# Kernel tuning notes

Hardware: AMD Instinct MI355X
Metric: run time of the kernel (lower is better)

Reference implementation:

```python
import jax, jax.numpy as jnp
import numpy as np
import math

E, NNODE = 32768, 2048          # edges, nodes
NUM_SPECIES, EMB = 100, 32
MUL, HIDDEN, N_RBF, LMAX, ENV_P = 16, 256, 8, 3, 6
SL = {0: slice(0, 1), 1: slice(1, 4), 2: slice(4, 9), 3: slice(9, 16)}  # SH blocks


def _cg(j1, m1, j2, m2, j3, m3):
    """Clebsch-Gordan coefficient (Racah formula), complex SH basis."""
    if m1 + m2 != m3:
        return 0.0
    f = math.factorial
    pre = math.sqrt((2*j3+1) * f(j1+j2-j3) * f(j1-j2+j3) * f(-j1+j2+j3) / f(j1+j2+j3+1))
    pre *= math.sqrt(f(j3+m3)*f(j3-m3)*f(j1-m1)*f(j1+m1)*f(j2-m2)*f(j2+m2))
    s = 0.0
    kmin = max(0, j2 - j3 - m1, j1 - j3 + m2)
    kmax = min(j1 + j2 - j3, j1 - m1, j2 + m2)
    for k in range(kmin, kmax + 1):
        s += (-1)**k / (f(k)*f(j1+j2-j3-k)*f(j1-m1-k)*f(j2+m2-k)*f(j3-j2+m1+k)*f(j3-j1-m2+k))
    return pre * s


def _umat(l):
    """Complex->real spherical-harmonics change of basis."""
    U = np.zeros((2*l+1, 2*l+1), dtype=complex)
    U[l, l] = 1.0
    s2 = 1.0 / math.sqrt(2.0)
    for m in range(1, l + 1):
        U[l+m, l-m] = s2
        U[l+m, l+m] = (-1)**m * s2
        U[l-m, l-m] = 1j * s2
        U[l-m, l+m] = -1j * (-1)**m * s2
    return U


def _real_coupling(l1, l2, l3):
    """Real-basis CG coupling tensor, Frobenius-normalized (w3j analogue)."""
    C = np.zeros((2*l1+1, 2*l2+1, 2*l3+1), dtype=complex)
    for a, m1 in enumerate(range(-l1, l1+1)):
        for b, m2 in enumerate(range(-l2, l2+1)):
            for c, m3 in enumerate(range(-l3, l3+1)):
                C[a, b, c] = _cg(l1, m1, l2, m2, l3, m3)
    T = np.einsum('am,bn,ck,mnk->abc', _umat(l1), _umat(l2), _umat(l3).conj(), C)
    Tr, Ti = np.real(T), np.imag(T)
    T = Tr if np.linalg.norm(Tr) >= np.linalg.norm(Ti) else Ti
    n = np.linalg.norm(T)
    return None if n < 1e-8 else (T / n).astype(np.float32)


PATHS = {l3: [] for l3 in range(LMAX + 1)}
for _l1 in range(LMAX + 1):
    for _l2 in range(LMAX + 1):
        for _l3 in range(abs(_l1 - _l2), min(_l1 + _l2, LMAX) + 1):
            _T = _real_coupling(_l1, _l2, _l3)
            if _T is not None:
                PATHS[_l3].append((_l1, _l2, jnp.asarray(_T)))
NPATH = {l3: len(PATHS[l3]) for l3 in range(LMAX + 1)}


def envelope(d):  # polynomial smoothing envelope, p=6, cutoff=1
    p = ENV_P
    e = 1.0 - 0.5*(p+1)*(p+2)*d**p + p*(p+2)*d**(p+1) - 0.5*p*(p+1)*d**(p+2)
    return jnp.where(d < 1.0, e, 0.0)


def bessel(d):  # radial Bessel basis [E] -> [E, N_RBF]
    n = jnp.arange(1, N_RBF + 1, dtype=d.dtype)
    ds = jnp.where(d == 0.0, 1.0, d)[:, None]
    return (math.sqrt(2.0) * jnp.sin(n * jnp.pi * ds) / ds) * envelope(d)[:, None]


def sph_harm16(u):  # real SH l=0..3, component norm (|Y_l|^2 = 2l+1), [E,16]
    x, y, z = u[:, 0], u[:, 1], u[:, 2]
    x2, y2, z2 = x*x, y*y, z*z
    s3, s15, s5 = math.sqrt(3.0), math.sqrt(15.0), math.sqrt(5.0)
    s358, s105 = math.sqrt(35.0/8.0), math.sqrt(105.0)
    s218, s7 = math.sqrt(21.0/8.0), math.sqrt(7.0)
    return jnp.stack([
        jnp.ones_like(x),
        s3*y, s3*z, s3*x,
        s15*x*y, s15*y*z, 0.5*s5*(3*z2 - 1), s15*x*z, 0.5*s15*(x2 - y2),
        s358*y*(3*x2 - y2), s105*x*y*z, s218*y*(5*z2 - 1), 0.5*s7*(5*z2 - 3)*z,
        s218*x*(5*z2 - 1), 0.5*s105*(x2 - y2)*z, s358*x*(x2 - y2),
    ], axis=1)


def dense(x, W):  # e3nn-style bias-free linear, 1/sqrt(fan_in)
    return (x @ W) / math.sqrt(W.shape[0])


def dense_axis(V, W):  # [E,C,K] x [C,D] -> [E,D,K]
    return jnp.einsum('eck,cd->edk', V, W) / math.sqrt(W.shape[0])


def tensor_product(A, B, lmax_out):
    """CG tensor product [E,MUL,16] x [E,MUL,16] -> {l3: [E,MUL*npath,2l3+1]}."""
    out = {}
    for l3 in range(lmax_out + 1):
        scale = math.sqrt(2*l3 + 1)
        parts = [scale * jnp.einsum('ijk,emi,emj->emk', T, A[:, :, SL[l1]], B[:, :, SL[l2]])
                 for (l1, l2, T) in PATHS[l3]]
        out[l3] = jnp.concatenate(parts, axis=1)
    return out


def allegro_layer(x, V, Y, senders, eps, env, alpha, Ww, Wl, Wv):
    w = dense(x, Ww)                                          # [E,MUL]
    node = jax.ops.segment_sum(w[:, :, None] * Y[:, None, :], senders, num_segments=NNODE)
    wY = node[senders] * eps                                  # scatter_sum + map_back
    lmax_out = LMAX if Wv is not None else 0
    tp = tensor_product(wY, V, lmax_out)
    xc = jnp.concatenate([x, tp[0][:, :, 0]], axis=1)         # fold 0e into scalars
    h = jax.nn.silu(dense(xc, Wl[0]))
    h = jax.nn.silu(dense(h, Wl[1]))
    y = env[:, None] * dense(h, Wl[2])
    a2 = alpha**2
    x = (x + a2 * y) / (1.0 + a2)
    if Wv is None:
        return x, None
    Vn = jnp.concatenate(
        [jnp.zeros((V.shape[0], MUL, 1), x.dtype)] +           # no 0e in output irreps
        [dense_axis(tp[l], Wv[l - 1]) for l in (1, 2, 3)], axis=2)
    return x, Vn


def _forward(vectors, varepsilon, alpha, emb, W_tb1, W_tb2, W_tb3, W_tb4,
             W_w0, W_w1, W_l11, W_l12, W_l13, W_v1, W_v2, W_v3,
             W_w2, W_l21, W_l22, W_l23, W_h, W_out,
             senders, receivers, species):
    d = jnp.linalg.norm(vectors, axis=1)
    u = vectors / jnp.where(d == 0.0, 1.0, d)[:, None]
    env = envelope(d)
    eps = 1.0 / jnp.sqrt(1.0 + varepsilon**2)
    x = jnp.concatenate([bessel(d), emb[species[senders]], emb[species[receivers]]], axis=1)
    x = jnp.where(d[:, None] == 0.0, 0.0, x)
    x = jax.nn.silu(dense(x, W_tb1))
    x = jax.nn.silu(dense(x, W_tb2))
    x = jax.nn.silu(dense(x, W_tb3))
    x = dense(x, W_tb4)
    x = env[:, None] * x                                      # [E,HIDDEN]
    Y = sph_harm16(u)                                         # [E,16]
    V = dense(x, W_w0)[:, :, None] * Y[:, None, :]            # [E,MUL,16]
    x, V = allegro_layer(x, V, Y, senders, eps, env, alpha,
                         W_w1, (W_l11, W_l12, W_l13), (W_v1, W_v2, W_v3))
    x, _ = allegro_layer(x, V, Y, senders, eps, env, alpha,
                         W_w2, (W_l21, W_l22, W_l23), None)
    x = dense(x, W_h)
    return env[:, None] * dense(x, W_out)                     # [E,1]


def setup_inputs():
    key = jax.random.key(0)
    ks = jax.random.split(key, 32)
    dirs = jax.random.normal(ks[0], (E, 3), dtype=jnp.float32)
    dirs = dirs / jnp.linalg.norm(dirs, axis=1, keepdims=True)
    r = jax.random.uniform(ks[1], (E, 1), minval=0.05, maxval=0.95, dtype=jnp.float32)
    w = lambda k, s: jax.random.normal(k, s, dtype=jnp.float32)
    n0 = NPATH[0]
    return {
        "vectors": dirs * r,
        "varepsilon": jnp.asarray(4.0, jnp.float32),   # sqrt(avg_num_neighbors=16)
        "alpha": jnp.asarray(1.0, jnp.float32),
        "emb": w(ks[5], (NUM_SPECIES, EMB)),
        "W_tb1": w(ks[6], (N_RBF + 2*EMB, HIDDEN // 8)),
        "W_tb2": w(ks[7], (HIDDEN // 8, HIDDEN // 4)),
        "W_tb3": w(ks[8], (HIDDEN // 4, HIDDEN // 2)),
        "W_tb4": w(ks[9], (HIDDEN // 2, HIDDEN)),
        "W_w0": w(ks[10], (HIDDEN, MUL)),
        "W_w1": w(ks[11], (HIDDEN, MUL)),
        "W_l11": w(ks[12], (HIDDEN + MUL * n0, HIDDEN)),
        "W_l12": w(ks[13], (HIDDEN, HIDDEN)),
        "W_l13": w(ks[14], (HIDDEN, HIDDEN)),
        "W_v1": w(ks[15], (MUL * NPATH[1], MUL)),
        "W_v2": w(ks[16], (MUL * NPATH[2], MUL)),
        "W_v3": w(ks[17], (MUL * NPATH[3], MUL)),
        "W_w2": w(ks[18], (HIDDEN, MUL)),
        "W_l21": w(ks[19], (HIDDEN + MUL * n0, HIDDEN)),
        "W_l22": w(ks[20], (HIDDEN, HIDDEN)),
        "W_l23": w(ks[21], (HIDDEN, HIDDEN)),
        "W_h": w(ks[22], (HIDDEN, 128)),
        "W_out": w(ks[23], (128, 1)),
        "senders": jax.random.randint(ks[2], (E,), 0, NNODE),
        "receivers": jax.random.randint(ks[3], (E,), 0, NNODE),
        "species": jax.random.randint(ks[4], (NNODE,), 0, NUM_SPECIES),
    }


def reference(vectors, varepsilon, alpha, emb, W_tb1, W_tb2, W_tb3, W_tb4,
              W_w0, W_w1, W_l11, W_l12, W_l13, W_v1, W_v2, W_v3,
              W_w2, W_l21, W_l22, W_l23, W_h, W_out,
              senders, receivers, species):
    return _forward(vectors, varepsilon, alpha, emb, W_tb1, W_tb2, W_tb3, W_tb4,
                    W_w0, W_w1, W_l11, W_l12, W_l13, W_v1, W_v2, W_v3,
                    W_w2, W_l21, W_l22, W_l23, W_h, W_out,
                    senders, receivers, species)
```

## Files before the change

kernel.cpp:

```cpp
#include <hip/hip_runtime.h>
#include <cmath>
#include <complex>
#include <cstdio>
#include <cstring>
#include <algorithm>

#define E_EDGES 32768
#define NNODES  2048
#define VN_E    128

namespace cgt {

static double fct(int n){
  static const double f[13] = {1.,1.,2.,6.,24.,120.,720.,5040.,40320.,362880.,
                               3628800.,39916800.,479001600.};
  return f[n];
}

static double cg(int j1,int m1,int j2,int m2,int j3,int m3){
  if (m1+m2 != m3) return 0.0;
  double pre = std::sqrt((2*j3+1)*fct(j1+j2-j3)*fct(j1-j2+j3)*fct(-j1+j2+j3)/fct(j1+j2+j3+1));
  pre *= std::sqrt(fct(j3+m3)*fct(j3-m3)*fct(j1-m1)*fct(j1+m1)*fct(j2-m2)*fct(j2+m2));
  int kmin = 0;
  if (j2-j3-m1 > kmin) kmin = j2-j3-m1;
// ... 301 lines not shown
        int row = mrow + r4 + r;
        HsA[row*264 + j*16 + fr] = f2h(silu(acc[j][r]*rs));
      }
    __syncthreads();
  }

  {
    f32x4 acc[16] = {};
    for (int k0 = 0; k0 < 128; k0 += 32) {
#pragma unroll
      for (int h = 0; h < 2; h++) {
        int n = h*128 + srb;
        const unsigned short* s = Wt4 + (size_t)n*128 + k0 + skb;
        uint4 u0 = *(const uint4*)s;
        uint4 u1 = *(const uint4*)(s + 8);
        *(uint4*)((char*)BsB + swz(n, skb))     = u0;
        *(uint4*)((char*)BsB + swz(n, skb + 8)) = u1;
      }
      __syncthreads();
      half8 af = *(half8*)(HsA + (mrow + fr)*264 + k0 + fk);
#pragma unroll
      for (int j = 0; j < 16; j++) {
        half8 bf = *(half8*)((char*)BsB + swz(j*16 + fr, fk));
        acc[j] = MFMA16(af, bf, acc[j], 0, 0, 0);
      }
      __syncthreads();
    }
    const float rs = 0.08838834764831845f;
#pragma unroll
    for (int j = 0; j < 16; j++)
#pragma unroll
      for (int r = 0; r < 4; r++) {
        int row = mrow + r4 + r;
        float v = acc[j][r]*rs*envb[bm + row];
        unsigned short hv = f2h(v);
        HsB[row*264 + j*16 + fr] = hv;
        Xout[((size_t)(bm + row))*256 + j*16 + fr] = hv;
      }
    __syncthreads();
  }

  {
    f32x4 acc[2] = {};
    for (int k0 = 0; k0 < 256; k0 += 32) {
      if (tid < 64) {
        int n = tid >> 1, kb = (tid & 1) * 16;
        const unsigned short* s = Wt01 + (size_t)n*256 + k0 + kb;
        uint4 u0 = *(const uint4*)s;
        uint4 u1 = *(const uint4*)(s + 8);
        *(uint4*)((char*)BsB + swz(n, kb))     = u0;
        *(uint4*)((char*)BsB + swz(n, kb + 8)) = u1;
      }
      __syncthreads();
      half8 af = *(half8*)(HsB + (mrow + fr)*264 + k0 + fk);
      half8 b0 = *(half8*)((char*)BsB + swz(fr, fk));
      half8 b1 = *(half8*)((char*)BsB + swz(16 + fr, fk));
      acc[0] = MFMA16(af, b0, acc[0], 0, 0, 0);
      acc[1] = MFMA16(af, b1, acc[1], 0, 0, 0);
      __syncthreads();
    }
#pragma unroll
    for (int r = 0; r < 4; r++) {
      int row = mrow + r4 + r;
      w0s[row*16 + fr] = acc[0][r]*0.0625f;
      wb[((size_t)(bm + row))*16 + fr] = acc[1][r]*0.0625f;
    }
    __syncthreads();
  }

  for (int i = tid; i < 64*256; i += 256) {
    int e = i >> 8, idx = i & 255;
    V[(((size_t)(bm + e)) << 8) + idx] =
        f2h(w0s[e*16 + (idx & 15)] * Yb[(bm + e)*16 + (idx >> 4)]);
  }
}

template<int MODE>
__global__ __launch_bounds__(512) void mlp3_k(
    const unsigned short* __restrict__ X, const unsigned short* __restrict__ T0,
    const unsigned short* __restrict__ W1t, const unsigned short* __restrict__ W2t,
    const unsigned short* __restrict__ W3t, unsigned short* __restrict__ Out,
    const float* __restrict__ env, const float* __restrict__ alphap,
    const unsigned short* __restrict__ Wtw2, float* __restrict__ wb,
    const float* __restrict__ hc, float* __restrict__ outE)
{
  __shared__ unsigned short AsB[128*32];
  __shared__ unsigned short BsB[256*32];
  __shared__ unsigned short Hs[128*264];
  __shared__ float hcs[256];
  __shared__ float red[512];
  const int tid  = threadIdx.x;
  const int wave = tid >> 6, lane = tid & 63;
  const int bm = blockIdx.x*128;
  const int rowh = (wave >> 2)*64;
  const int wc = (wave & 3)*64;
  const int fr = lane & 15, fk = (lane >> 4) * 8;
  const int r4 = (lane >> 4) << 2;
  const int sra = tid >> 2, ska = (tid & 3) * 8;
  const int srb = tid >> 1, skb = (tid & 1) * 16;
  if (MODE == 1 && tid < 256) hcs[tid] = hc[tid];
  f32x4 acc[4][4] = {};

  for (int k0 = 0; k0 < 320; k0 += 32) {
    {
      int kk = k0 + ska;
      const unsigned short* ap = (kk < 256)
        ? X  + (size_t)(bm + sra)*256 + kk
        : T0 + (size_t)(bm + sra)*64  + (kk - 256);
      *(uint4*)((char*)AsB + swz(sra, ska)) = *(const uint4*)ap;
    }
    {
      const unsigned short* s = W1t + (size_t)srb*320 + k0 + skb;
      *(uint4*)((char*)BsB + swz(srb, skb))     = *(const uint4*)s;
      *(uint4*)((char*)BsB + swz(srb, skb + 8)) = *(const uint4*)(s + 8);
    }
    __syncthreads();
    half8 af[4], bf[4];
#pragma unroll
    for (int i = 0; i < 4; i++)
      af[i] = *(half8*)((char*)AsB + swz(rowh + i*16 + fr, fk));
#pragma unroll
    for (int j = 0; j < 4; j++)
      bf[j] = *(half8*)((char*)BsB + swz(wc + j*16 + fr, fk));
#pragma unroll
    for (int i = 0; i < 4; i++)
#pragma unroll
      for (int j = 0; j < 4; j++)
        acc[i][j] = MFMA16(af[i], bf[j], acc[i][j], 0, 0, 0);
    __syncthreads();
  }
  const float rs320 = 0.055901699437494740f;
#pragma unroll
  for (int i = 0; i < 4; i++)
#pragma unroll
    for (int r = 0; r < 4; r++) {
      int row = rowh + i*16 + r4 + r;
#pragma unroll
      for (int j = 0; j < 4; j++) {
        Hs[row*264 + wc + j*16 + fr] = f2h(silu(acc[i][j][r]*rs320));
        acc[i][j][r] = 0.f;
      }
    }
  __syncthreads();

  for (int k0 = 0; k0 < 256; k0 += 32) {
    {
      const unsigned short* s = W2t + (size_t)srb*256 + k0 + skb;
      *(uint4*)((char*)BsB + swz(srb, skb))     = *(const uint4*)s;
      *(uint4*)((char*)BsB + swz(srb, skb + 8)) = *(const uint4*)(s + 8);
    }
    __syncthreads();
    half8 af[4], bf[4];
#pragma unroll
    for (int i = 0; i < 4; i++)
      af[i] = *(half8*)(Hs + (rowh + i*16 + fr)*264 + k0 + fk);
#pragma unroll
    for (int j = 0; j < 4; j++)
      bf[j] = *(half8*)((char*)BsB + swz(wc + j*16 + fr, fk));
#pragma unroll
    for (int i = 0; i < 4; i++)
#pragma unroll
      for (int j = 0; j < 4; j++)
        acc[i][j] = MFMA16(af[i], bf[j], acc[i][j], 0, 0, 0);
    __syncthreads();
  }
#pragma unroll
  for (int i = 0; i < 4; i++)
#pragma unroll
    for (int r = 0; r < 4; r++) {
      int row = rowh + i*16 + r4 + r;
#pragma unroll
      for (int j = 0; j < 4; j++) {
        Hs[row*264 + wc + j*16 + fr] = f2h(silu(acc[i][j][r]*0.0625f));
        acc[i][j][r] = 0.f;
      }
    }
  __syncthreads();

  for (int k0 = 0; k0 < 256; k0 += 32) {
    {
      const unsigned short* s = W3t + (size_t)srb*256 + k0 + skb;
      *(uint4*)((char*)BsB + swz(srb, skb))     = *(const uint4*)s;
      *(uint4*)((char*)BsB + swz(srb, skb + 8)) = *(const uint4*)(s + 8);
    }
    __syncthreads();
    half8 af[4], bf[4];
#pragma unroll
    for (int i = 0; i < 4; i++)
      af[i] = *(half8*)(Hs + (rowh + i*16 + fr)*264 + k0 + fk);
#pragma unroll
    for (int j = 0; j < 4; j++)
      bf[j] = *(half8*)((char*)BsB + swz(wc + j*16 + fr, fk));
#pragma unroll
    for (int i = 0; i < 4; i++)
#pragma unroll
      for (int j = 0; j < 4; j++)
        acc[i][j] = MFMA16(af[i], bf[j], acc[i][j], 0, 0, 0);
    __syncthreads();
  }
  {
    float al = alphap[0];
    float a2 = al*al, inv1a2 = 1.f/(1.f+a2);
#pragma unroll
    for (int i = 0; i < 4; i++)
#pragma unroll
      for (int r = 0; r < 4; r++) {
        int row = rowh + i*16 + r4 + r;
        int grow = bm + row;
        float ev = env[grow];
#pragma unroll
        for (int j = 0; j < 4; j++) {
          int col = wc + j*16 + fr;
          float v = acc[i][j][r]*0.0625f*ev;
          v = (h2f(X[(size_t)grow*256 + col]) + a2*v)*inv1a2;
          unsigned short hv = f2h(v);
          Hs[row*264 + col] = hv;
          if (MODE == 0) Out[(size_t)grow*256 + col] = hv;
        }
      }
  }
  __syncthreads();

  if (MODE == 0) {
    f32x4 acc2[4] = {};
    for (int k0 = 0; k0 < 256; k0 += 32) {
      if (tid < 32) {
        int n = tid >> 1, kb = (tid & 1) * 16;
        const unsigned short* s = Wtw2 + (size_t)n*256 + k0 + kb;
        *(uint4*)((char*)BsB + swz(n, kb))     = *(const uint4*)s;
        *(uint4*)((char*)BsB + swz(n, kb + 8)) = *(const uint4*)(s + 8);
      }
      __syncthreads();
      if ((wave & 3) == 0) {
        half8 bf = *(half8*)((char*)BsB + swz(fr, fk));
#pragma unroll
        for (int i = 0; i < 4; i++) {
          half8 af = *(half8*)(Hs + (rowh + i*16 + fr)*264 + k0 + fk);
          acc2[i] = MFMA16(af, bf, acc2[i], 0, 0, 0);
        }
      }
      __syncthreads();
    }
    if ((wave & 3) == 0) {
#pragma unroll
      for (int i = 0; i < 4; i++)
#pragma unroll
        for (int r = 0; r < 4; r++)
          wb[((size_t)(bm + rowh + i*16 + r4 + r))*16 + fr] = acc2[i][r]*0.0625f;
    }
  } else {
    int row = tid >> 2, q = tid & 3;
    float p = 0.f;
#pragma unroll 16
    for (int c = q*64; c < q*64 + 64; c++)
      p += h2f(Hs[row*264 + c]) * hcs[c];
    red[tid] = p;
    __syncthreads();
    if (q == 0) {
      float t = red[tid] + red[tid+1] + red[tid+2] + red[tid+3];
      outE[bm + row] = env[bm + row]*t*0.0055242717280199023f;
    }
  }
}

__global__ __launch_bounds__(512) void vn_k(
    const float* __restrict__ node, const unsigned short* __restrict__ V,
    const int* __restrict__ senders, const float* __restrict__ varepsp,
    const int* __restrict__ pairsG, const unsigned short* __restrict__ Gtt,
    unsigned short* __restrict__ Vn, int Kdim,
    const int* __restrict__ pmeta, const int* __restrict__ entIJ,
    const float* __restrict__ entVal, unsigned short* __restrict__ tp0)
{
  __shared__ unsigned short Ab[VN_E*264];
  __shared__ unsigned short Bb[VN_E*264];
  __shared__ int Ps[256];
  const int tid = threadIdx.x;
  const int e0 = blockIdx.x * VN_E;
  const int wave = tid >> 6, lane = tid & 63;
  float ve = varepsp[0];
  float eps = rsqrtf(1.f + ve*ve);
  if (tid < 256) Ps[tid] = pairsG[tid];
#pragma unroll
  for (int rr = 0; rr < 16; rr++) {
    int row = wave*16 + rr;
    int s = senders[e0 + row];
    float4 fa = *(const float4*)(node + ((size_t)s << 8) + 4*lane);
    uint2 ub = *(const uint2*)(V + (((size_t)(e0 + row)) << 8) + 4*lane);
    unsigned short* ad = Ab + row*264 + 4*lane;
    unsigned short* bd = Bb + row*264 + 4*lane;
    uint2 ua;
    ua.x = (unsigned)f2h(fa.x*eps) | ((unsigned)f2h(fa.y*eps) << 16);
    ua.y = (unsigned)f2h(fa.z*eps) | ((unsigned)f2h(fa.w*eps) << 16);
    *(uint2*)ad = ua;
    *(uint2*)bd = ub;
  }
  __syncthreads();
  for (int o = tid; o < VN_E*64; o += 512) {
    int e = o >> 6, c = o & 63;
    int p = c >> 4, m = c & 15;
    const unsigned short* Ae = Ab + e*264;
    const unsigned short* Be = Bb + e*264;
    int es = pmeta[p*4+1], ec = pmeta[p*4+2];
    float acc = 0.f;
    for (int t = 0; t < ec; t++) {
      int ij = entIJ[es+t];
      acc += entVal[es+t] * h2f(Ae[((ij&255)<<4)+m]) * h2f(Be[(((ij>>8)&255)<<4)+m]);
    }
    tp0[((size_t)(e0+e)<<6) + pmeta[p*4+0] + m] = f2h(acc);
  }
  const int rowb = (wave & 1) * 64;
  const int wc   = (wave >> 1) * 64;
  const int fr = lane & 15, fk = (lane >> 4) * 8;
  const int pairSel = fk >> 4;
  const int moff = fk & 15;
  const int nslab = Kdim >> 5;
  f32x4 acc[4][4] = {};

  const unsigned short* Ar0 = Ab + (rowb + fr)*264;
  const unsigned short* Br0 = Bb + (rowb + fr)*264;
  const unsigned short* Ar1 = Ab + (rowb + 16 + fr)*264;
  const unsigned short* Br1 = Bb + (rowb + 16 + fr)*264;
  const unsigned short* Ar2 = Ab + (rowb + 32 + fr)*264;
  const unsigned short* Br2 = Bb + (rowb + 32 + fr)*264;
  const unsigned short* Ar3 = Ab + (rowb + 48 + fr)*264;
  const unsigned short* Br3 = Bb + (rowb + 48 + fr)*264;

// ... 27 lines not shown
    half8 a1 = rA1 * rB1;
    half8 a2 = rA2 * rB2;
    half8 a3 = rA3 * rB3;
    if (sl + 1 < nslab) {
      int pn = Ps[2*(sl + 1) + pairSel];
      int aoffn = ((pn & 255) << 4) + moff;
      int boffn = (((pn >> 8) & 255) << 4) + moff;
      rA0 = *(const half8*)(Ar0 + aoffn);
      rB0 = *(const half8*)(Br0 + boffn);
      rA1 = *(const half8*)(Ar1 + aoffn);
      rB1 = *(const half8*)(Br1 + boffn);
      rA2 = *(const half8*)(Ar2 + aoffn);
      rB2 = *(const half8*)(Br2 + boffn);
      rA3 = *(const half8*)(Ar3 + aoffn);
      rB3 = *(const half8*)(Br3 + boffn);
    }
    half8 d0, d1, d2, d3;
    if (sl + 2 < nslab) {
      const unsigned short* gn = gp + (size_t)(sl + 2) * 8192;
      d0 = *(const half8*)(gn);
      d1 = *(const half8*)(gn + 512);
      d2 = *(const half8*)(gn + 1024);
      d3 = *(const half8*)(gn + 1536);
    } else { d0 = c0; d1 = c1; d2 = c2; d3 = c3; }
    acc[0][0] = MFMA16(a0, b0, acc[0][0], 0, 0, 0);
    acc[1][0] = MFMA16(a1, b0, acc[1][0], 0, 0, 0);
    acc[2][0] = MFMA16(a2, b0, acc[2][0], 0, 0, 0);
    acc[3][0] = MFMA16(a3, b0, acc[3][0], 0, 0, 0);
    acc[0][1] = MFMA16(a0, b1, acc[0][1], 0, 0, 0);
    acc[1][1] = MFMA16(a1, b1, acc[1][1], 0, 0, 0);
    acc[2][1] = MFMA16(a2, b1, acc[2][1], 0, 0, 0);
    acc[3][1] = MFMA16(a3, b1, acc[3][1], 0, 0, 0);
    acc[0][2] = MFMA16(a0, b2, acc[0][2], 0, 0, 0);
    acc[1][2] = MFMA16(a1, b2, acc[1][2], 0, 0, 0);
    acc[2][2] = MFMA16(a2, b2, acc[2][2], 0, 0, 0);
    acc[3][2] = MFMA16(a3, b2, acc[3][2], 0, 0, 0);
    acc[0][3] = MFMA16(a0, b3, acc[0][3], 0, 0, 0);
    acc[1][3] = MFMA16(a1, b3, acc[1][3], 0, 0, 0);
    acc[2][3] = MFMA16(a2, b3, acc[2][3], 0, 0, 0);
    acc[3][3] = MFMA16(a3, b3, acc[3][3], 0, 0, 0);
    b0 = c0; b1 = c1; b2 = c2; b3 = c3;
    c0 = d0; c1 = d1; c2 = d2; c3 = d3;
  }
  const int r4 = (lane >> 4) << 2;
#pragma unroll
  for (int rg = 0; rg < 4; rg++) {
#pragma unroll
    for (int j = 0; j < 4; j++) {
#pragma unroll
      for (int r = 0; r < 4; r++) {
        int row = e0 + rowb + rg*16 + r4 + r;
        int col = wc + j*16 + fr;
        Vn[(size_t)row*256 + col] = f2h(acc[rg][j][r]);
      }
    }
  }
}

__global__ void gbuild_k(const float* __restrict__ TD,
    const float* __restrict__ Wv1, const float* __restrict__ Wv2,
    const float* __restrict__ Wv3, const int* __restrict__ sl_origc,
    unsigned short* __restrict__ Gt, int Kdim, int npairs,
    int s1b, int s1e, int s2e, int s3e)
{
  int k = blockIdx.x*256 + threadIdx.x;
  if (k >= Kdim) return;
  int col = blockIdx.y;
  int pair = k >> 4, m = k & 15;
  int d = col & 15, kabs = col >> 4;
  float acc = 0.f;
  if (kabs > 0 && pair < npairs) {
    const float* Wv; int ss, se, kloc;
    if (kabs < 4)      { Wv = Wv1; ss = s1b; se = s1e; kloc = kabs - 1; }
    else if (kabs < 9) { Wv = Wv2; ss = s1e; se = s2e; kloc = kabs - 4; }
    else               { Wv = Wv3; ss = s2e; se = s3e; kloc = kabs - 9; }
    for (int slot = ss; slot < se; slot++)
      acc += TD[((pair*30) + (slot - 4))*8 + kloc] * Wv[(sl_origc[slot] + m)*16 + d];
    acc *= rsqrtf((float)(16*(se - ss)));
  }
  Gt[((size_t)((k >> 5)*256 + col))*32 + (k & 31)] = f2h(acc);
}

struct WDesc { const float* src; unsigned short* dst; int K; int lgN; };
struct WPack { WDesc d[11]; };
__global__ void wcvt_k(WPack p){
  WDesc d = p.d[blockIdx.y];
  int total = d.K << d.lgN;
  int gid = blockIdx.x*256 + threadIdx.x;
  if (gid >= total) return;
  int k = gid >> d.lgN, n = gid & ((1 << d.lgN) - 1);
  d.dst[(size_t)n*d.K + k] = f2h(d.src[gid]);
}

__global__ void wcvt01_k(const float* __restrict__ W0, const float* __restrict__ W1,
                         unsigned short* __restrict__ dst){
  int gid = blockIdx.x*256 + threadIdx.x;
  int k = gid >> 5, n = gid & 31;
  float v = (n < 16) ? W0[k*16 + n] : W1[k*16 + (n - 16)];
  dst[(size_t)n*256 + k] = f2h(v);
}

__global__ void whc_k(const float* __restrict__ Wh, const float* __restrict__ Wout,
                      float* __restrict__ hc)
{
  int k = threadIdx.x;
  float s = 0.f;
#pragma unroll 16
  for (int j = 0; j < 128; j++) s += Wh[k*128 + j] * Wout[j];
  hc[k] = s;
}

__global__ void edge_init_k(const float* __restrict__ vectors, const int* __restrict__ senders,
    const int* __restrict__ receivers, const int* __restrict__ species,
    const float* __restrict__ emb, float* __restrict__ envb, float* __restrict__ Yb,
    float* __restrict__ x72)
{
  const int e = blockIdx.x*256 + threadIdx.x;
  float vx = vectors[e*3+0], vy = vectors[e*3+1], vz = vectors[e*3+2];
  float d = sqrtf(vx*vx+vy*vy+vz*vz);
  float dd = (d==0.f) ? 1.f : d;
  float invd = 1.f/dd;
  float x = vx*invd, y = vy*invd, z = vz*invd;
  float d2=d*d, d3=d2*d, d6=d3*d3, d7=d6*d, d8=d7*d;
  float envv = (d<1.f) ? (1.f - 28.f*d6 + 48.f*d7 - 21.f*d8) : 0.f;
  envb[e] = envv;
  float mask = (d==0.f)?0.f:1.f;
  const float SQ2 = 1.41421356237309515f;
  const float PIf = 3.14159265358979323846f;
  float* xr = x72 + (size_t)e*72;
#pragma unroll
  for (int n=1;n<=8;n++)
    xr[n-1] = SQ2 * sinf((float)n*PIf*dd)*invd*envv*mask;
  int sp_s = species[senders[e]], sp_r = species[receivers[e]];
  const float* es_ = emb + (size_t)sp_s*32;
  const float* er_ = emb + (size_t)sp_r*32;
#pragma unroll 8
  for (int k=0;k<32;k++){ xr[8+k] = es_[k]*mask; xr[40+k] = er_[k]*mask; }
  float x2=x*x, y2=y*y, z2=z*z;
  const float s3=1.7320508075688772f, s15=3.872983346207417f, s5=2.23606797749979f;
  const float s358=2.0916500663351889f, s105=10.246950765959598f;
  const float s218=1.6201851746019651f, s7=2.6457513110645907f;
  float* Yr = Yb + ((size_t)e<<4);
  Yr[0]=1.f;           Yr[1]=s3*y;          Yr[2]=s3*z;           Yr[3]=s3*x;
  Yr[4]=s15*x*y;       Yr[5]=s15*y*z;       Yr[6]=0.5f*s5*(3.f*z2-1.f);
  Yr[7]=s15*x*z;       Yr[8]=0.5f*s15*(x2-y2);
  Yr[9]=s358*y*(3.f*x2-y2);  Yr[10]=s105*x*y*z;  Yr[11]=s218*y*(5.f*z2-1.f);
  Yr[12]=0.5f*s7*(5.f*z2-3.f)*z;  Yr[13]=s218*x*(5.f*z2-1.f);
  Yr[14]=0.5f*s105*(x2-y2)*z;     Yr[15]=s358*x*(x2-y2);
}

__global__ void hist_k(const int* __restrict__ senders, int* cnt){
  int e = blockIdx.x*256 + threadIdx.x;
  atomicAdd(&cnt[senders[e]], 1);
}

__global__ void scan_k(const int* __restrict__ cnt, int* __restrict__ starts,
                       int* __restrict__ cursor){
  __shared__ int s[NNODES];
  const int tid = threadIdx.x;
  for (int i = tid; i < NNODES; i += 256) s[i] = cnt[i];
  __syncthreads();
  if (tid == 0) {
    int run = 0;
    for (int i = 0; i < NNODES; i++) { int c = s[i]; s[i] = run; run += c; }
  }
  __syncthreads();
  for (int i = tid; i < NNODES; i += 256) { starts[i] = s[i]; cursor[i] = s[i]; }
  if (tid == 0) starts[NNODES] = E_EDGES;
}

__global__ void perm_k(const int* __restrict__ senders, int* cursor,
                       int* __restrict__ perm){
  int e = blockIdx.x*256 + threadIdx.x;
  int pos = atomicAdd(&cursor[senders[e]], 1);
  perm[pos] = e;
}

__global__ __launch_bounds__(256) void nodesum_k(const float* __restrict__ w,
    const float* __restrict__ Y, const int* __restrict__ perm,
    const int* __restrict__ starts, float* __restrict__ node)
{
  __shared__ float buf[8*32];
  const int n = blockIdx.x;
  const int tid = threadIdx.x;
  const int s0 = starts[n], s1 = starts[n+1];
  const int a = tid >> 4, m = tid & 15;
  float acc = 0.f;
  for (int i = s0; i < s1; i += 8) {
    int nb = s1 - i; if (nb > 8) nb = 8;
    int slot = tid >> 5, comp = tid & 31;
    if (slot < nb) {
      int e = perm[i + slot];
      buf[slot*32 + comp] = (comp < 16) ? w[(e<<4)+comp] : Y[(e<<4)+comp-16];
    }
    __syncthreads();
    for (int q = 0; q < nb; q++)
      acc += buf[q*32 + m] * buf[q*32 + 16 + a];
    __syncthreads();
  }
  node[((size_t)n<<8) + tid] = acc;
}

__global__ void tp2_k(const float* __restrict__ node, const unsigned short* __restrict__ Vn,
    const int* __restrict__ senders, const float* __restrict__ varepsp,
    const int* __restrict__ pmeta, const int* __restrict__ entIJ,
    const float* __restrict__ entVal, unsigned short* __restrict__ tp0)
{
  const int gid = blockIdx.x*256 + threadIdx.x;
  const int e = gid >> 6, c = gid & 63;
  const int p = c >> 4, m = c & 15;
  float ve = varepsp[0];
  float eps = rsqrtf(1.f + ve*ve);
  int s = senders[e];
  const float* Am = &node[((size_t)s<<8)];
  const unsigned short* Bm = &Vn[((size_t)e<<8)];
  int es = pmeta[p*4+1], ec = pmeta[p*4+2];
  float acc = 0.f;
  for (int t=0;t<ec;t++){
    int ij = entIJ[es+t];
    acc += entVal[es+t] * Am[((ij&255)<<4) + m] * h2f(Bm[(((ij>>8)&255)<<4) + m]);
  }
  tp0[((size_t)e<<6) + pmeta[p*4+0] + m] = f2h(acc * eps);
}


extern "C" void kernel_launch(void* const* d_in, const int* in_sizes, int n_in,
                              void* d_out, int out_size, void* d_ws, size_t ws_size,
                              hipStream_t stream)
{
  const float* vectors = (const float*)d_in[0];
  const float* vareps  = (const float*)d_in[1];
  const float* alpha   = (const float*)d_in[2];
  const float* emb     = (const float*)d_in[3];
  const float* W_tb1   = (const float*)d_in[4];
  const float* W_tb2   = (const float*)d_in[5];
  const float* W_tb3   = (const float*)d_in[6];
  const float* W_tb4   = (const float*)d_in[7];
  const float* W_w0    = (const float*)d_in[8];
  const float* W_w1    = (const float*)d_in[9];
  const float* W_l11   = (const float*)d_in[10];
  const float* W_l12   = (const float*)d_in[11];
  const float* W_l13   = (const float*)d_in[12];
  const float* W_v1    = (const float*)d_in[13];
  const float* W_v2    = (const float*)d_in[14];
  const float* W_v3    = (const float*)d_in[15];
  const float* W_w2    = (const float*)d_in[16];
  const float* W_l21   = (const float*)d_in[17];
  const float* W_l22   = (const float*)d_in[18];
  const float* W_l23   = (const float*)d_in[19];
  const float* W_h     = (const float*)d_in[20];
  const float* W_out   = (const float*)d_in[21];
  const int* senders   = (const int*)d_in[22];
  const int* receivers = (const int*)d_in[23];
  const int* species   = (const int*)d_in[24];

  static cgt::Tables tb;
  cgt::build(tb);
  const int Kdim = tb.npairs * 16;

  char* ws = (char*)d_ws;
  size_t off = 0;
  auto alloc = [&](size_t bytes)->void*{
    void* p = ws + off; off += (bytes + 255) & ~(size_t)255; return p;
  };
  float* t_val = (float*)alloc(sizeof(tb.val));
  int*   t_ij  = (int*)  alloc(sizeof(tb.ij));
  int*   t_pm  = (int*)  alloc(sizeof(tb.pmeta));
  float* t_td  = (float*)alloc(sizeof(tb.TD));
  int*   t_pr  = (int*)  alloc(sizeof(tb.pairs));
  int*   t_oc  = (int*)  alloc(sizeof(tb.sl_origc));
  float* envb  = (float*)alloc((size_t)E_EDGES*4);
  float* Yb    = (float*)alloc((size_t)E_EDGES*16*4);
  float* xb    = (float*)alloc((size_t)E_EDGES*256*4);
  float* Vb    = (float*)alloc((size_t)E_EDGES*256*4);
  float* bufA  = (float*)alloc((size_t)E_EDGES*72*4);
  float* wb    = (float*)alloc((size_t)E_EDGES*16*4);
  float* tp0b  = (float*)alloc((size_t)E_EDGES*64*4);
  float* nodeb = (float*)alloc((size_t)NNODES*256*4);
  float* hcb   = (float*)alloc(256*4);
  int* cntb    = (int*)alloc(NNODES*4);
  int* startsb = (int*)alloc((NNODES+1)*4);
  int* cursorb = (int*)alloc(NNODES*4);
  int* permb   = (int*)alloc(E_EDGES*4);
  unsigned short* Gt = (unsigned short*)alloc((size_t)256*Kdim*2);
  unsigned short* Wt_tb1 = (unsigned short*)alloc(32*72*2);
  unsigned short* Wt_tb2 = (unsigned short*)alloc(64*32*2);
  unsigned short* Wt_tb3 = (unsigned short*)alloc(128*64*2);
  unsigned short* Wt_tb4 = (unsigned short*)alloc(256*128*2);
  unsigned short* Wt_w01 = (unsigned short*)alloc(32*256*2);
  unsigned short* Wt_w2  = (unsigned short*)alloc(16*256*2);
  unsigned short* Wt_l11 = (unsigned short*)alloc(320*256*2);
  unsigned short* Wt_l12 = (unsigned short*)alloc(256*256*2);
  unsigned short* Wt_l13 = (unsigned short*)alloc(256*256*2);
  unsigned short* Wt_l21 = (unsigned short*)alloc(320*256*2);
  unsigned short* Wt_l22 = (unsigned short*)alloc(256*256*2);
  unsigned short* Wt_l23 = (unsigned short*)alloc(256*256*2);
  if (off > ws_size) {
    fprintf(stderr, "[allegro] workspace too small: need %zu, have %zu\n", off, ws_size);
    return;
  }
  unsigned short* xb16 = (unsigned short*)xb;
  unsigned short* tp016 = (unsigned short*)tp0b;
  unsigned short* V16 = (unsigned short*)Vb;

  hipMemcpyAsync(t_val, tb.val,     sizeof(tb.val),     hipMemcpyHostToDevice, stream);
  hipMemcpyAsync(t_ij,  tb.ij,      sizeof(tb.ij),      hipMemcpyHostToDevice, stream);
  hipMemcpyAsync(t_pm,  tb.pmeta,   sizeof(tb.pmeta),   hipMemcpyHostToDevice, stream);
  hipMemcpyAsync(t_td,  tb.TD,      sizeof(tb.TD),      hipMemcpyHostToDevice, stream);
  hipMemcpyAsync(t_pr,  tb.pairs,   sizeof(tb.pairs),   hipMemcpyHostToDevice, stream);
  hipMemcpyAsync(t_oc,  tb.sl_origc,sizeof(tb.sl_origc),hipMemcpyHostToDevice, stream);

  const int s1b = tb.l3np[0];
  const int s1e = s1b + tb.l3np[1];
  const int s2e = s1e + tb.l3np[2];
  const int s3e = s2e + tb.l3np[3];

  {
    dim3 g((Kdim + 255)/256, 256);
    gbuild_k<<<g, 256, 0, stream>>>(t_td, W_v1, W_v2, W_v3, t_oc, Gt, Kdim,
                                    tb.npairs, s1b, s1e, s2e, s3e);
  }
  {
    WPack p;
    p.d[0]  = { W_tb1, Wt_tb1,  72, 5 };
    p.d[1]  = { W_tb2, Wt_tb2,  32, 6 };
    p.d[2]  = { W_tb3, Wt_tb3,  64, 7 };
    p.d[3]  = { W_tb4, Wt_tb4, 128, 8 };
    p.d[4]  = { W_l11, Wt_l11, 320, 8 };
    p.d[5]  = { W_l12, Wt_l12, 256, 8 };
    p.d[6]  = { W_l13, Wt_l13, 256, 8 };
    p.d[7]  = { W_l21, Wt_l21, 320, 8 };
    p.d[8]  = { W_l22, Wt_l22, 256, 8 };
    p.d[9]  = { W_l23, Wt_l23, 256, 8 };
    p.d[10] = { W_w2,  Wt_w2,  256, 4 };
    dim3 g(320, 11);
    wcvt_k<<<g, 256, 0, stream>>>(p);
  }
  wcvt01_k<<<32, 256, 0, stream>>>(W_w0, W_w1, Wt_w01);
  whc_k<<<1, 256, 0, stream>>>(W_h, W_out, hcb);

  hipMemsetAsync(cntb, 0, NNODES*4, stream);
  hist_k<<<E_EDGES/256, 256, 0, stream>>>(senders, cntb);
  scan_k<<<1, 256, 0, stream>>>(cntb, startsb, cursorb);
  perm_k<<<E_EDGES/256, 256, 0, stream>>>(senders, cursorb, permb);

  edge_init_k<<<E_EDGES/256, 256, 0, stream>>>(vectors, senders, receivers, species,
                                               emb, envb, Yb, bufA);
  tb_fused_k<<<E_EDGES/64, 256, 0, stream>>>(bufA, Wt_tb1, Wt_tb2, Wt_tb3, Wt_tb4,
                                             Wt_w01, Yb, envb, xb16, V16, wb);

  nodesum_k<<<NNODES, 256, 0, stream>>>(wb, Yb, permb, startsb, nodeb);
  vn_k<<<E_EDGES/VN_E, 512, 0, stream>>>(nodeb, V16, senders, vareps, t_pr, Gt,
                                         V16, Kdim, t_pm, t_ij, t_val, tp016);
  mlp3_k<0><<<E_EDGES/128, 512, 0, stream>>>(xb16, tp016, Wt_l11, Wt_l12, Wt_l13,
                                             xb16, envb, alpha, Wt_w2, wb,
                                             nullptr, nullptr);

  nodesum_k<<<NNODES, 256, 0, stream>>>(wb, Yb, permb, startsb, nodeb);
  tp2_k<<<E_EDGES*64/256, 256, 0, stream>>>(nodeb, V16, senders, vareps, t_pm, t_ij,
                                            t_val, tp016);
  mlp3_k<1><<<E_EDGES/128, 512, 0, stream>>>(xb16, tp016, Wt_l21, Wt_l22, Wt_l23,
                                             nullptr, envb, alpha, nullptr, nullptr,
                                             hcb, (float*)d_out);
}
```

Before: 388.0 us.

## Stream MLP weights from pre-tiled global layout into registers, fuse sort and head prep

The three-layer MLP kernel no longer stages A and B tiles through shared memory with barriers. Weights are pre-converted into a k-slab tiled layout and loaded straight into registers with one-slab-ahead prefetch. The first-layer activations are also read directly from global memory. The histogram, scan and permutation kernels are merged into a single one-block kernel using shared-memory atomics, and the head-vector kernel is folded into the second MLP launch. Together these cut launches and LDS barriers, at the cost of more global and L2 traffic per wave and a serial single-block sort.

Result: slower. 402.4 us, median of 3 (+3.7%).

```diff
diff --git a/kernel.cpp b/kernel.cpp
--- a/kernel.cpp
+++ b/kernel.cpp
@@ -407,10 +407,9 @@
     const unsigned short* __restrict__ W3t, unsigned short* __restrict__ Out,
     const float* __restrict__ env, const float* __restrict__ alphap,
     const unsigned short* __restrict__ Wtw2, float* __restrict__ wb,
-    const float* __restrict__ hc, float* __restrict__ outE)
+    const float* __restrict__ Wh, const float* __restrict__ Wout,
+    float* __restrict__ outE)
 {
-  __shared__ unsigned short AsB[128*32];
-  __shared__ unsigned short BsB[256*32];
   __shared__ unsigned short Hs[128*264];
   __shared__ float hcs[256];
   __shared__ float red[512];
@@ -421,38 +420,54 @@
   const int wc = (wave & 3)*64;
   const int fr = lane & 15, fk = (lane >> 4) * 8;
   const int r4 = (lane >> 4) << 2;
-  const int sra = tid >> 2, ska = (tid & 3) * 8;
-  const int srb = tid >> 1, skb = (tid & 1) * 16;
-  if (MODE == 1 && tid < 256) hcs[tid] = hc[tid];
+  if (MODE == 1 && tid < 256) {
+    float s = 0.f;
+#pragma unroll 16
+    for (int j = 0; j < 128; j++) s += Wh[tid*128 + j] * Wout[j];
+    hcs[tid] = s;
+  }
   f32x4 acc[4][4] = {};
 
-  for (int k0 = 0; k0 < 320; k0 += 32) {
-    {
-      int kk = k0 + ska;
-      const unsigned short* ap = (kk < 256)
-        ? X  + (size_t)(bm + sra)*256 + kk
-        : T0 + (size_t)(bm + sra)*64  + (kk - 256);
-      *(uint4*)((char*)AsB + swz(sra, ska)) = *(const uint4*)ap;
-    }
-    {
-      const unsigned short* s = W1t + (size_t)srb*320 + k0 + skb;
-      *(uint4*)((char*)BsB + swz(srb, skb))     = *(const uint4*)s;
-      *(uint4*)((char*)BsB + swz(srb, skb + 8)) = *(const uint4*)(s + 8);
-    }
-    __syncthreads();
-    half8 af[4], bf[4];
-#pragma unroll
-    for (int i = 0; i < 4; i++)
-      af[i] = *(half8*)((char*)AsB + swz(rowh + i*16 + fr, fk));
-#pragma unroll
-    for (int j = 0; j < 4; j++)
-      bf[j] = *(half8*)((char*)BsB + swz(wc + j*16 + fr, fk));
-#pragma unroll
-    for (int i = 0; i < 4; i++)
-#pragma unroll
-      for (int j = 0; j < 4; j++)
-        acc[i][j] = MFMA16(af[i], bf[j], acc[i][j], 0, 0, 0);
-    __syncthreads();
+  {
+    const unsigned short* bp = W1t + ((size_t)(wc + fr))*32 + fk;
+    #define LDA1(i,k0) (*((const half8*)(((k0)+fk < 256) \
+        ? X  + (size_t)(bm + rowh + (i)*16 + fr)*256 + (k0) + fk \
+        : T0 + (size_t)(bm + rowh + (i)*16 + fr)*64  + (k0) + fk - 256)))
+    half8 a0 = LDA1(0,0), a1 = LDA1(1,0), a2 = LDA1(2,0), a3 = LDA1(3,0);
+    half8 b0 = *(const half8*)(bp);
+    half8 b1 = *(const half8*)(bp + 512);
+    half8 b2 = *(const half8*)(bp + 1024);
+    half8 b3 = *(const half8*)(bp + 1536);
+    for (int sl = 0; sl < 10; sl++) {
+      half8 na0, na1, na2, na3, nb0, nb1, nb2, nb3;
+      if (sl + 1 < 10) {
+        int k0n = (sl + 1)*32;
+        na0 = LDA1(0,k0n); na1 = LDA1(1,k0n); na2 = LDA1(2,k0n); na3 = LDA1(3,k0n);
+        const unsigned short* bn = bp + (size_t)(sl + 1)*8192;
+        nb0 = *(const half8*)(bn);
+        nb1 = *(const half8*)(bn + 512);
+        nb2 = *(const half8*)(bn + 1024);
+        nb3 = *(const half8*)(bn + 1536);
+      } else { na0=a0; na1=a1; na2=a2; na3=a3; nb0=b0; nb1=b1; nb2=b2; nb3=b3; }
+      acc[0][0] = MFMA16(a0, b0, acc[0][0], 0, 0, 0);
+      acc[1][0] = MFMA16(a1, b0, acc[1][0], 0, 0, 0);
+      acc[2][0] = MFMA16(a2, b0, acc[2][0], 0, 0, 0);
+      acc[3][0] = MFMA16(a3, b0, acc[3][0], 0, 0, 0);
+      acc[0][1] = MFMA16(a0, b1, acc[0][1], 0, 0, 0);
+      acc[1][1] = MFMA16(a1, b1, acc[1][1], 0, 0, 0);
+      acc[2][1] = MFMA16(a2, b1, acc[2][1], 0, 0, 0);
+      acc[3][1] = MFMA16(a3, b1, acc[3][1], 0, 0, 0);
+      acc[0][2] = MFMA16(a0, b2, acc[0][2], 0, 0, 0);
+      acc[1][2] = MFMA16(a1, b2, acc[1][2], 0, 0, 0);
+      acc[2][2] = MFMA16(a2, b2, acc[2][2], 0, 0, 0);
+      acc[3][2] = MFMA16(a3, b2, acc[3][2], 0, 0, 0);
+      acc[0][3] = MFMA16(a0, b3, acc[0][3], 0, 0, 0);
+      acc[1][3] = MFMA16(a1, b3, acc[1][3], 0, 0, 0);
+      acc[2][3] = MFMA16(a2, b3, acc[2][3], 0, 0, 0);
+      acc[3][3] = MFMA16(a3, b3, acc[3][3], 0, 0, 0);
+      a0=na0; a1=na1; a2=na2; a3=na3; b0=nb0; b1=nb1; b2=nb2; b3=nb3;
+    }
+    #undef LDA1
   }
   const float rs320 = 0.055901699437494740f;
 #pragma unroll
@@ -468,27 +483,46 @@
     }
   __syncthreads();
 
-  for (int k0 = 0; k0 < 256; k0 += 32) {
-    {
-      const unsigned short* s = W2t + (size_t)srb*256 + k0 + skb;
-      *(uint4*)((char*)BsB + swz(srb, skb))     = *(const uint4*)s;
-      *(uint4*)((char*)BsB + swz(srb, skb + 8)) = *(const uint4*)(s + 8);
-    }
-    __syncthreads();
-    half8 af[4], bf[4];
-#pragma unroll
-    for (int i = 0; i < 4; i++)
-      af[i] = *(half8*)(Hs + (rowh + i*16 + fr)*264 + k0 + fk);
-#pragma unroll
-    for (int j = 0; j < 4; j++)
-      bf[j] = *(half8*)((char*)BsB + swz(wc + j*16 + fr, fk));
-#pragma unroll
-    for (int i = 0; i < 4; i++)
-#pragma unroll
-      for (int j = 0; j < 4; j++)
-        acc[i][j] = MFMA16(af[i], bf[j], acc[i][j], 0, 0, 0);
-    __syncthreads();
-  }
+  {
+    const unsigned short* bp = W2t + ((size_t)(wc + fr))*32 + fk;
+    half8 b0 = *(const half8*)(bp);
+    half8 b1 = *(const half8*)(bp + 512);
+    half8 b2 = *(const half8*)(bp + 1024);
+    half8 b3 = *(const half8*)(bp + 1536);
+    for (int sl = 0; sl < 8; sl++) {
+      half8 nb0, nb1, nb2, nb3;
+      if (sl + 1 < 8) {
+        const unsigned short* bn = bp + (size_t)(sl + 1)*8192;
+        nb0 = *(const half8*)(bn);
+        nb1 = *(const half8*)(bn + 512);
+        nb2 = *(const half8*)(bn + 1024);
+        nb3 = *(const half8*)(bn + 1536);
+      } else { nb0=b0; nb1=b1; nb2=b2; nb3=b3; }
+      int k0 = sl*32;
+      half8 a0 = *(half8*)(Hs + (rowh +  0 + fr)*264 + k0 + fk);
+      half8 a1 = *(half8*)(Hs + (rowh + 16 + fr)*264 + k0 + fk);
+      half8 a2 = *(half8*)(Hs + (rowh + 32 + fr)*264 + k0 + fk);
+      half8 a3 = *(half8*)(Hs + (rowh + 48 + fr)*264 + k0 + fk);
+      acc[0][0] = MFMA16(a0, b0, acc[0][0], 0, 0, 0);
+      acc[1][0] = MFMA16(a1, b0, acc[1][0], 0, 0, 0);
+      acc[2][0] = MFMA16(a2, b0, acc[2][0], 0, 0, 0);
+      acc[3][0] = MFMA16(a3, b0, acc[3][0], 0, 0, 0);
+      acc[0][1] = MFMA16(a0, b1, acc[0][1], 0, 0, 0);
+      acc[1][1] = MFMA16(a1, b1, acc[1][1], 0, 0, 0);
+      acc[2][1] = MFMA16(a2, b1, acc[2][1], 0, 0, 0);
+      acc[3][1] = MFMA16(a3, b1, acc[3][1], 0, 0, 0);
+      acc[0][2] = MFMA16(a0, b2, acc[0][2], 0, 0, 0);
+      acc[1][2] = MFMA16(a1, b2, acc[1][2], 0, 0, 0);
+      acc[2][2] = MFMA16(a2, b2, acc[2][2], 0, 0, 0);
+      acc[3][2] = MFMA16(a3, b2, acc[3][2], 0, 0, 0);
+      acc[0][3] = MFMA16(a0, b3, acc[0][3], 0, 0, 0);
+      acc[1][3] = MFMA16(a1, b3, acc[1][3], 0, 0, 0);
+      acc[2][3] = MFMA16(a2, b3, acc[2][3], 0, 0, 0);
+      acc[3][3] = MFMA16(a3, b3, acc[3][3], 0, 0, 0);
+      b0=nb0; b1=nb1; b2=nb2; b3=nb3;
+    }
+  }
+  __syncthreads();
 #pragma unroll
   for (int i = 0; i < 4; i++)
 #pragma unroll
@@ -502,27 +536,46 @@
     }
   __syncthreads();
 
-  for (int k0 = 0; k0 < 256; k0 += 32) {
-    {
-      const unsigned short* s = W3t + (size_t)srb*256 + k0 + skb;
-      *(uint4*)((char*)BsB + swz(srb, skb))     = *(const uint4*)s;
-      *(uint4*)((char*)BsB + swz(srb, skb + 8)) = *(const uint4*)(s + 8);
-    }
-    __syncthreads();
-    half8 af[4], bf[4];
-#pragma unroll
-    for (int i = 0; i < 4; i++)
-      af[i] = *(half8*)(Hs + (rowh + i*16 + fr)*264 + k0 + fk);
-#pragma unroll
-    for (int j = 0; j < 4; j++)
-      bf[j] = *(half8*)((char*)BsB + swz(wc + j*16 + fr, fk));
-#pragma unroll
-    for (int i = 0; i < 4; i++)
-#pragma unroll
-      for (int j = 0; j < 4; j++)
-        acc[i][j] = MFMA16(af[i], bf[j], acc[i][j], 0, 0, 0);
-    __syncthreads();
-  }
+  {
+    const unsigned short* bp = W3t + ((size_t)(wc + fr))*32 + fk;
+    half8 b0 = *(const half8*)(bp);
+    half8 b1 = *(const half8*)(bp + 512);
+    half8 b2 = *(const half8*)(bp + 1024);
+    half8 b3 = *(const half8*)(bp + 1536);
+    for (int sl = 0; sl < 8; sl++) {
+      half8 nb0, nb1, nb2, nb3;
+      if (sl + 1 < 8) {
+        const unsigned short* bn = bp + (size_t)(sl + 1)*8192;
+        nb0 = *(const half8*)(bn);
+        nb1 = *(const half8*)(bn + 512);
+        nb2 = *(const half8*)(bn + 1024);
+        nb3 = *(const half8*)(bn + 1536);
+      } else { nb0=b0; nb1=b1; nb2=b2; nb3=b3; }
+      int k0 = sl*32;
+      half8 a0 = *(half8*)(Hs + (rowh +  0 + fr)*264 + k0 + fk);
+      half8 a1 = *(half8*)(Hs + (rowh + 16 + fr)*264 + k0 + fk);
+      half8 a2 = *(half8*)(Hs + (rowh + 32 + fr)*264 + k0 + fk);
+      half8 a3 = *(half8*)(Hs + (rowh + 48 + fr)*264 + k0 + fk);
+      acc[0][0] = MFMA16(a0, b0, acc[0][0], 0, 0, 0);
+      acc[1][0] = MFMA16(a1, b0, acc[1][0], 0, 0, 0);
+      acc[2][0] = MFMA16(a2, b0, acc[2][0], 0, 0, 0);
+      acc[3][0] = MFMA16(a3, b0, acc[3][0], 0, 0, 0);
+      acc[0][1] = MFMA16(a0, b1, acc[0][1], 0, 0, 0);
+      acc[1][1] = MFMA16(a1, b1, acc[1][1], 0, 0, 0);
+      acc[2][1] = MFMA16(a2, b1, acc[2][1], 0, 0, 0);
+      acc[3][1] = MFMA16(a3, b1, acc[3][1], 0, 0, 0);
+      acc[0][2] = MFMA16(a0, b2, acc[0][2], 0, 0, 0);
+      acc[1][2] = MFMA16(a1, b2, acc[1][2], 0, 0, 0);
+      acc[2][2] = MFMA16(a2, b2, acc[2][2], 0, 0, 0);
+      acc[3][2] = MFMA16(a3, b2, acc[3][2], 0, 0, 0);
+      acc[0][3] = MFMA16(a0, b3, acc[0][3], 0, 0, 0);
+      acc[1][3] = MFMA16(a1, b3, acc[1][3], 0, 0, 0);
+      acc[2][3] = MFMA16(a2, b3, acc[2][3], 0, 0, 0);
+      acc[3][3] = MFMA16(a3, b3, acc[3][3], 0, 0, 0);
+      b0=nb0; b1=nb1; b2=nb2; b3=nb3;
+    }
+  }
+  __syncthreads();
   {
     float al = alphap[0];
     float a2 = al*al, inv1a2 = 1.f/(1.f+a2);
@@ -547,26 +600,20 @@
   __syncthreads();
 
   if (MODE == 0) {
-    f32x4 acc2[4] = {};
-    for (int k0 = 0; k0 < 256; k0 += 32) {
-      if (tid < 32) {
-        int n = tid >> 1, kb = (tid & 1) * 16;
-        const unsigned short* s = Wtw2 + (size_t)n*256 + k0 + kb;
-        *(uint4*)((char*)BsB + swz(n, kb))     = *(const uint4*)s;
-        *(uint4*)((char*)BsB + swz(n, kb + 8)) = *(const uint4*)(s + 8);
-      }
-      __syncthreads();
-      if ((wave & 3) == 0) {
-        half8 bf = *(half8*)((char*)BsB + swz(fr, fk));
+    if ((wave & 3) == 0) {
+      f32x4 acc2[4] = {};
+      const unsigned short* bp = Wtw2 + ((size_t)fr)*32 + fk;
+      half8 bf = *(const half8*)(bp);
+      for (int sl = 0; sl < 8; sl++) {
+        half8 nbf = (sl + 1 < 8) ? *(const half8*)(bp + (size_t)(sl + 1)*512) : bf;
+        int k0 = sl*32;
 #pragma unroll
         for (int i = 0; i < 4; i++) {
           half8 af = *(half8*)(Hs + (rowh + i*16 + fr)*264 + k0 + fk);
           acc2[i] = MFMA16(af, bf, acc2[i], 0, 0, 0);
         }
-      }
-      __syncthreads();
-    }
-    if ((wave & 3) == 0) {
+        bf = nbf;
+      }
 #pragma unroll
       for (int i = 0; i < 4; i++)
 #pragma unroll
@@ -760,7 +807,7 @@
 }
 
 struct WDesc { const float* src; unsigned short* dst; int K; int lgN; };
-struct WPack { WDesc d[11]; };
+struct WPack { WDesc d[4]; };
 __global__ void wcvt_k(WPack p){
   WDesc d = p.d[blockIdx.y];
   int total = d.K << d.lgN;
@@ -770,22 +817,22 @@
   d.dst[(size_t)n*d.K + k] = f2h(d.src[gid]);
 }
 
+struct WPackT { WDesc d[7]; };
+__global__ void wcvt_tile_k(WPackT p){
+  WDesc d = p.d[blockIdx.y];
+  int total = d.K << d.lgN;
+  int gid = blockIdx.x*256 + threadIdx.x;
+  if (gid >= total) return;
+  int k = gid >> d.lgN, n = gid & ((1 << d.lgN) - 1);
+  d.dst[(((size_t)(k >> 5) << d.lgN) + n)*32 + (k & 31)] = f2h(d.src[gid]);
+}
+
 __global__ void wcvt01_k(const float* __restrict__ W0, const float* __restrict__ W1,
                          unsigned short* __restrict__ dst){
   int gid = blockIdx.x*256 + threadIdx.x;
   int k = gid >> 5, n = gid & 31;
   float v = (n < 16) ? W0[k*16 + n] : W1[k*16 + (n - 16)];
   dst[(size_t)n*256 + k] = f2h(v);
-}
-
-__global__ void whc_k(const float* __restrict__ Wh, const float* __restrict__ Wout,
-                      float* __restrict__ hc)
-{
-  int k = threadIdx.x;
-  float s = 0.f;
-#pragma unroll 16
-  for (int j = 0; j < 128; j++) s += Wh[k*128 + j] * Wout[j];
-  hc[k] = s;
 }
 
 __global__ void edge_init_k(const float* __restrict__ vectors, const int* __restrict__ senders,
@@ -827,31 +874,39 @@
   Yr[14]=0.5f*s105*(x2-y2)*z;     Yr[15]=s358*x*(x2-y2);
 }
 
-__global__ void hist_k(const int* __restrict__ senders, int* cnt){
-  int e = blockIdx.x*256 + threadIdx.x;
-  atomicAdd(&cnt[senders[e]], 1);
-}
-
-__global__ void scan_k(const int* __restrict__ cnt, int* __restrict__ starts,
-                       int* __restrict__ cursor){
-  __shared__ int s[NNODES];
+__global__ __launch_bounds__(1024) void sortprep_k(const int* __restrict__ senders,
+    int* __restrict__ starts, int* __restrict__ perm)
+{
+  __shared__ int cnt[NNODES];
+  __shared__ int csum[64];
   const int tid = threadIdx.x;
-  for (int i = tid; i < NNODES; i += 256) s[i] = cnt[i];
+  for (int i = tid; i < NNODES; i += 1024) cnt[i] = 0;
+  __syncthreads();
+  for (int e = tid; e < E_EDGES; e += 1024) atomicAdd(&cnt[senders[e]], 1);
+  __syncthreads();
+  if (tid < 64) {
+    int s = 0;
+    for (int i = 0; i < 32; i++) s += cnt[tid*32 + i];
+    csum[tid] = s;
+  }
   __syncthreads();
   if (tid == 0) {
     int run = 0;
-    for (int i = 0; i < NNODES; i++) { int c = s[i]; s[i] = run; run += c; }
-  }
-  __syncthreads();
-  for (int i = tid; i < NNODES; i += 256) { starts[i] = s[i]; cursor[i] = s[i]; }
+    for (int i = 0; i < 64; i++) { int c = csum[i]; csum[i] = run; run += c; }
+  }
+  __syncthreads();
+  if (tid < 64) {
+    int run = csum[tid];
+    for (int i = 0; i < 32; i++) { int c = cnt[tid*32 + i]; cnt[tid*32 + i] = run; run += c; }
+  }
+  __syncthreads();
+  for (int i = tid; i < NNODES; i += 1024) starts[i] = cnt[i];
   if (tid == 0) starts[NNODES] = E_EDGES;
-}
-
-__global__ void perm_k(const int* __restrict__ senders, int* cursor,
-                       int* __restrict__ perm){
-  int e = blockIdx.x*256 + threadIdx.x;
-  int pos = atomicAdd(&cursor[senders[e]], 1);
-  perm[pos] = e;
+  __syncthreads();
+  for (int e = tid; e < E_EDGES; e += 1024) {
+    int pos = atomicAdd(&cnt[senders[e]], 1);
+    perm[pos] = e;
+  }
 }
 
 __global__ __launch_bounds__(256) void nodesum_k(const float* __restrict__ w,
@@ -955,10 +1010,7 @@
   float* wb    = (float*)alloc((size_t)E_EDGES*16*4);
   float* tp0b  = (float*)alloc((size_t)E_EDGES*64*4);
   float* nodeb = (float*)alloc((size_t)NNODES*256*4);
-  float* hcb   = (float*)alloc(256*4);
-  int* cntb    = (int*)alloc(NNODES*4);
   int* startsb = (int*)alloc((NNODES+1)*4);
-  int* cursorb = (int*)alloc(NNODES*4);
   int* permb   = (int*)alloc(E_EDGES*4);
   unsigned short* Gt = (unsigned short*)alloc((size_t)256*Kdim*2);
   unsigned short* Wt_tb1 = (unsigned short*)alloc(32*72*2);
@@ -1000,27 +1052,27 @@
   }
   {
     WPack p;
-    p.d[0]  = { W_tb1, Wt_tb1,  72, 5 };
-    p.d[1]  = { W_tb2, Wt_tb2,  32, 6 };
-    p.d[2]  = { W_tb3, Wt_tb3,  64, 7 };
-    p.d[3]  = { W_tb4, Wt_tb4, 128, 8 };
-    p.d[4]  = { W_l11, Wt_l11, 320, 8 };
-    p.d[5]  = { W_l12, Wt_l12, 256, 8 };
-    p.d[6]  = { W_l13, Wt_l13, 256, 8 };
-    p.d[7]  = { W_l21, Wt_l21, 320, 8 };
-    p.d[8]  = { W_l22, Wt_l22, 256, 8 };
-    p.d[9]  = { W_l23, Wt_l23, 256, 8 };
-    p.d[10] = { W_w2,  Wt_w2,  256, 4 };
-    dim3 g(320, 11);
+    p.d[0] = { W_tb1, Wt_tb1,  72, 5 };
+    p.d[1] = { W_tb2, Wt_tb2,  32, 6 };
+    p.d[2] = { W_tb3, Wt_tb3,  64, 7 };
+    p.d[3] = { W_tb4, Wt_tb4, 128, 8 };
+    dim3 g(128, 4);
     wcvt_k<<<g, 256, 0, stream>>>(p);
   }
+  {
+    WPackT p;
+    p.d[0] = { W_l11, Wt_l11, 320, 8 };
+    p.d[1] = { W_l12, Wt_l12, 256, 8 };
+    p.d[2] = { W_l13, Wt_l13, 256, 8 };
+    p.d[3] = { W_l21, Wt_l21, 320, 8 };
+    p.d[4] = { W_l22, Wt_l22, 256, 8 };
+    p.d[5] = { W_l23, Wt_l23, 256, 8 };
+    p.d[6] = { W_w2,  Wt_w2,  256, 4 };
+    dim3 g(320, 7);
+    wcvt_tile_k<<<g, 256, 0, stream>>>(p);
+  }
   wcvt01_k<<<32, 256, 0, stream>>>(W_w0, W_w1, Wt_w01);
-  whc_k<<<1, 256, 0, stream>>>(W_h, W_out, hcb);
-
-  hipMemsetAsync(cntb, 0, NNODES*4, stream);
-  hist_k<<<E_EDGES/256, 256, 0, stream>>>(senders, cntb);
-  scan_k<<<1, 256, 0, stream>>>(cntb, startsb, cursorb);
-  perm_k<<<E_EDGES/256, 256, 0, stream>>>(senders, cursorb, permb);
+  sortprep_k<<<1, 1024, 0, stream>>>(senders, startsb, permb);
 
   edge_init_k<<<E_EDGES/256, 256, 0, stream>>>(vectors, senders, receivers, species,
                                                emb, envb, Yb, bufA);
@@ -1032,12 +1084,12 @@
                                          V16, Kdim, t_pm, t_ij, t_val, tp016);
   mlp3_k<0><<<E_EDGES/128, 512, 0, stream>>>(xb16, tp016, Wt_l11, Wt_l12, Wt_l13,
                                              xb16, envb, alpha, Wt_w2, wb,
-                                             nullptr, nullptr);
+                                             nullptr, nullptr, nullptr);
 
   nodesum_k<<<NNODES, 256, 0, stream>>>(wb, Yb, permb, startsb, nodeb);
   tp2_k<<<E_EDGES*64/256, 256, 0, stream>>>(nodeb, V16, senders, vareps, t_pm, t_ij,
                                             t_val, tp016);
   mlp3_k<1><<<E_EDGES/128, 512, 0, stream>>>(xb16, tp016, Wt_l21, Wt_l22, Wt_l23,
                                              nullptr, envb, alpha, nullptr, nullptr,
-                                             hcb, (float*)d_out);
-}
+                                             W_h, W_out, (float*)d_out);
+}
```
